# Performance work log

Hardware: AMD Instinct MI355X
Metric: run time of the kernel (lower is better)

## Reference

```python
import jax, jax.numpy as jnp
import numpy as np

B, S, HID = 1, 2048, 4096
H, KV, D = 32, 8, 128          # query heads, kv heads, head_dim
THETA = 100000.0               # rope base


def setup_inputs() -> dict:
    key = jax.random.key(0)
    k1, k2, k3, k4, k5 = jax.random.split(key, 5)
    hidden_states = jax.random.normal(k1, (B, S, HID), jnp.float32)
    # W_pack: Linear(hidden, H*D + 2*KV*D), torch weight layout [out, in]
    w_pack = jax.random.normal(k2, (H * D + 2 * KV * D, HID), jnp.float32) * 0.02
    w_o = jax.random.normal(k3, (HID, H * D), jnp.float32) * 0.02
    # conv kernels: per-kv-head causal mixing weights of width 2 (softmax-normalized at init)
    conv_k = jax.nn.softmax(jax.random.normal(k4, (KV, 2), jnp.float32), axis=-1)
    conv_v = jax.nn.softmax(jax.random.normal(k5, (KV, 2), jnp.float32), axis=-1)
    return dict(hidden_states=hidden_states, w_pack=w_pack, w_o=w_o,
                conv_k=conv_k, conv_v=conv_v)


def _causal_conv2(u, k):
    """u: [b,s,h,d], k: [h,2]. v[t] = k[h,0]*u[t-1] + k[h,1]*u[t] (zero pad at t=-1).
    Equivalent to custom_convolution with window 2 (unfold+mul+sum)."""
    prev = jnp.pad(u, ((0, 0), (1, 0), (0, 0), (0, 0)))[:, :-1]
    return k[None, None, :, 0:1] * prev + k[None, None, :, 1:2] * u


def _rope(x):
    """Non-interleaved (half-split) rotary over full head_dim. x: [b,s,h,d]."""
    s, d = x.shape[1], x.shape[-1]
    inv = 1.0 / (THETA ** (jnp.arange(0, d, 2, dtype=jnp.float32) / d))
    freqs = jnp.arange(s, dtype=jnp.float32)[:, None] * inv[None, :]  # [s, d/2]
    cos = jnp.cos(freqs)[None, :, None, :]
    sin = jnp.sin(freqs)[None, :, None, :]
    x1, x2 = x[..., : d // 2], x[..., d // 2:]
    return jnp.concatenate([x1 * cos - x2 * sin, x1 * sin + x2 * cos], axis=-1)


def reference(hidden_states, w_pack, w_o, conv_k, conv_v):
    qkv = hidden_states @ w_pack.T                       # [b,s,H*D+2*KV*D]
    q = qkv[..., : H * D].reshape(B, S, H, D)
    k = qkv[..., H * D: H * D + KV * D].reshape(B, S, KV, D)
    v = qkv[..., H * D + KV * D:].reshape(B, S, KV, D)

    # causal depthwise width-2 conv mixing on K and V (prefill path)
    k = _causal_conv2(k, conv_k)
    v = _causal_conv2(v, conv_v)

    # rotary on q, k
    q = _rope(q)
    k = _rope(k)

    # GQA: repeat kv heads to match query heads
    g = H // KV
    k = jnp.repeat(k, g, axis=2)
    v = jnp.repeat(v, g, axis=2)

    scale = 1.0 / np.sqrt(D).astype(np.float32)
    scores = jnp.einsum('bqhd,bkhd->bhqk', q, k) * scale  # [b,H,S,S]
    causal = jnp.tril(jnp.ones((S, S), dtype=bool))
    scores = jnp.where(causal[None, None], scores, jnp.finfo(scores.dtype).min)
    probs = jax.nn.softmax(scores, axis=-1)
    out = jnp.einsum('bhqk,bkhd->bqhd', probs, v).reshape(B, S, H * D)
    return out @ w_o.T
```

## Files before the change

kernel.cpp:

```cpp
#include <hip/hip_runtime.h>
#include <hip/hip_bf16.h>

#define S_LEN 2048
#define HID 4096
#define NH 32
#define NKV 8
#define HD 128

typedef unsigned short u16;
typedef __attribute__((ext_vector_type(4))) float f32x4;
typedef __attribute__((ext_vector_type(8))) short bf16x8;

__device__ __forceinline__ u16 f2bf(float x) {
  union { float f; unsigned u; } c; c.f = x;
  unsigned r = c.u + 0x7FFFu + ((c.u >> 16) & 1u);
  return (u16)(r >> 16);
}

__device__ __forceinline__ void gload16(const void* g, void* l) {
  __builtin_amdgcn_global_load_lds(
      (const __attribute__((address_space(1))) unsigned int*)g,
      (__attribute__((address_space(3))) unsigned int*)l, 16, 0, 0);
}

__global__ void cvt4_kernel(const float* __restrict__ s, u16* __restrict__ d, int n4) {
  int i = blockIdx.x * 256 + threadIdx.x;
  if (i >= n4) return;
  float4 v = ((const float4*)s)[i];
  ushort4 o;
  o.x = f2bf(v.x); o.y = f2bf(v.y); o.z = f2bf(v.z); o.w = f2bf(v.w);
  ((ushort4*)d)[i] = o;
}

__global__ void rope_tab_kernel(float2* __restrict__ tab) {
  int i = blockIdx.x * 256 + threadIdx.x;
  int t = i >> 6, d = i & 63;
  float inv = expf(-(float)d * (11.512925464970229f / 64.0f));
  float f = (float)t * inv;
  float2 cs; cs.x = cosf(f); cs.y = sinf(f);
  tab[i] = cs;
}

__global__ void rope_q_kernel(const float* __restrict__ qkv, const float2* __restrict__ tab,
                              u16* __restrict__ Q) {
  int i = blockIdx.x * 256 + threadIdx.x;
  int d = i & 63, h = (i >> 6) & 31, t = i >> 11;
  const float* row = qkv + (size_t)t * 6144 + h * 128;
  float x1 = row[d], x2 = row[d + 64];
  float2 cs = tab[(t << 6) | d];
  u16* orow = Q + (((size_t)t * NH + h) << 7);
  orow[d]      = f2bf(x1 * cs.x - x2 * cs.y);
  orow[d + 64] = f2bf(x1 * cs.y + x2 * cs.x);
}

__global__ void convrope_k_kernel(const float* __restrict__ qkv, const float* __restrict__ ck,
                                  const float2* __restrict__ tab, u16* __restrict__ K) {
  int i = blockIdx.x * 256 + threadIdx.x;
  int d = i & 63, kv = (i >> 6) & 7, t = i >> 9;
  const float* cur = qkv + (size_t)t * 6144 + 4096 + kv * 128;
  float c0 = ck[kv * 2], c1 = ck[kv * 2 + 1];
  float x1 = c1 * cur[d], x2 = c1 * cur[d + 64];
  if (t > 0) { const float* prv = cur - 6144; x1 += c0 * prv[d]; x2 += c0 * prv[d + 64]; }
  float2 cs = tab[(t << 6) | d];
  u16* orow = K + (((size_t)t * NKV + kv) << 7);
  orow[d]      = f2bf(x1 * cs.x - x2 * cs.y);
  orow[d + 64] = f2bf(x1 * cs.y + x2 * cs.x);
}

__global__ __launch_bounds__(256) void convT_v_kernel(const float* __restrict__ qkv,
                                                      const float* __restrict__ cv,
                                                      u16* __restrict__ VT) {
  __shared__ float ld[65][128];
  int tt = blockIdx.x * 64, kv = blockIdx.y;
  float c0 = cv[kv * 2], c1 = cv[kv * 2 + 1];
  for (int idx = threadIdx.x; idx < 65 * 128; idx += 256) {
    int r = idx >> 7, d = idx & 127;
    int t = tt - 1 + r;
    ld[r][d] = (t >= 0) ? qkv[(size_t)t * 6144 + 5120 + kv * 128 + d] : 0.f;
  }
  __syncthreads();
  int d = threadIdx.x >> 1, tc = (threadIdx.x & 1) * 32;
  u16* out = VT + ((size_t)kv * 128 + d) * S_LEN + tt + tc;
#pragma unroll
  for (int j = 0; j < 32; ++j)
    out[j] = f2bf(c0 * ld[tc + j][d] + c1 * ld[tc + j + 1][d]);
}

#define BM 128
#define BN 128
#define BK 64

__global__ __launch_bounds__(256, 2) void gemm_nt_kernel(const u16* __restrict__ A,
                                                         const u16* __restrict__ B,
                                                         float* __restrict__ C,
                                                         int M, int N, int K) {
  __shared__ __align__(16) u16 lA[BM * BK];
  __shared__ __align__(16) u16 lB[BN * BK];
  const int tid = threadIdx.x;
  const int wid = tid >> 6, lane = tid & 63;
  const int bm = blockIdx.y * BM, bn = blockIdx.x * BN;
  const int wr = (wid >> 1) * 64, wc = (wid & 1) * 64;
  const int lr = lane & 15, lg = lane >> 4;
  f32x4 acc[4][4] = {};
  const char* Ab = (const char*)A;
  const char* Bb = (const char*)B;
  const int nk = K / BK;
  for (int kt = 0; kt < nk; ++kt) {
    const size_t k0b = (size_t)kt * (BK * 2);
    __syncthreads();
#pragma unroll
    for (int i = 0; i < 4; ++i) {
      int off = (i * 4 + wid) * 1024 + lane * 16;
      int row = off >> 7, inrow = off & 127;
      int sw = inrow ^ ((row & 7) << 4);
      gload16(Ab + (size_t)(bm + row) * (K * 2) + k0b + sw, (char*)lA + (i * 4 + wid) * 1024);
      gload16(Bb + (size_t)(bn + row) * (K * 2) + k0b + sw, (char*)lB + (i * 4 + wid) * 1024);
    }
    __syncthreads();
    bf16x8 af[4][2], bfv[4][2];
#pragma unroll
    for (int m = 0; m < 4; ++m)
#pragma unroll
      for (int ks = 0; ks < 2; ++ks) {
        int row = wr + m * 16 + lr;
        int boff = row * 128 + ((ks * 64 + lg * 16) ^ ((row & 7) << 4));
        af[m][ks] = *(const bf16x8*)((const char*)lA + boff);
      }
#pragma unroll
    for (int n = 0; n < 4; ++n)
#pragma unroll
      for (int ks = 0; ks < 2; ++ks) {
        int row = wc + n * 16 + lr;
        int boff = row * 128 + ((ks * 64 + lg * 16) ^ ((row & 7) << 4));
        bfv[n][ks] = *(const bf16x8*)((const char*)lB + boff);
      }
#pragma unroll
    for (int m = 0; m < 4; ++m)
#pragma unroll
      for (int n = 0; n < 4; ++n)
#pragma unroll
        for (int ks = 0; ks < 2; ++ks)
          acc[m][n] = __builtin_amdgcn_mfma_f32_16x16x32_bf16(af[m][ks], bfv[n][ks], acc[m][n], 0, 0, 0);
  }
#pragma unroll
  for (int m = 0; m < 4; ++m)
#pragma unroll
    for (int n = 0; n < 4; ++n)
#pragma unroll
      for (int r = 0; r < 4; ++r) {
        int row = bm + wr + m * 16 + lg * 4 + r;
        int col = bn + wc + n * 16 + lr;
        C[(size_t)row * N + col] = acc[m][n][r];
      }
}

__global__ __launch_bounds__(256, 2) void attn_kernel(const u16* __restrict__ Q,
                                                      const u16* __restrict__ K,
                                                      const u16* __restrict__ VT,
                                                      u16* __restrict__ O) {
  __shared__ __align__(16) u16 lK[64 * 128];
  __shared__ __align__(16) u16 lV[128 * 64];
  __shared__ __align__(16) u16 lP[4][16 * 64];
  const int tid = threadIdx.x;
  const int wid = tid >> 6, lane = tid & 63;
  const int lr = lane & 15, lg = lane >> 4;
  const int qt = blockIdx.x, h = blockIdx.y;
  const int kvh = h >> 2;
  const int qrow = qt * 64 + wid * 16 + lr;

  bf16x8 qf[4];
#pragma unroll
  for (int ks = 0; ks < 4; ++ks)
    qf[ks] = *(const bf16x8*)(Q + (((size_t)qrow * NH + h) << 7) + ks * 32 + lg * 8);

  f32x4 o[8] = {};
  float mrow[4], lrow[4];
#pragma unroll
  for (int r = 0; r < 4; ++r) { mrow[r] = -1e30f; lrow[r] = 0.f; }

  const char* Kb = (const char*)K;
  const char* Vb = (const char*)VT;
  const float SC = 0.12752551286084f;

  for (int kt = 0; kt <= qt; ++kt) {
    __syncthreads();
#pragma unroll
    for (int i = 0; i < 4; ++i) {
      int off = (i * 4 + wid) * 1024 + lane * 16;
      int t = off >> 8, inrow = off & 255;
      gload16(Kb + (((size_t)((kt * 64 + t) * NKV + kvh)) << 8) + (inrow ^ ((t & 7) << 4)),
              (char*)lK + (i * 4 + wid) * 1024);
      int d = off >> 7, inr2 = off & 127;
      gload16(Vb + ((size_t)(kvh * 128 + d)) * (S_LEN * 2) + kt * 128 + (inr2 ^ ((d & 7) << 4)),
              (char*)lV + (i * 4 + wid) * 1024);
    }
    __syncthreads();

    f32x4 sv[4];
#pragma unroll
    for (int n = 0; n < 4; ++n) {
      f32x4 a = {};
#pragma unroll
      for (int ks = 0; ks < 4; ++ks) {
        int trow = n * 16 + lr;
        int boff = trow * 256 + ((ks * 64 + lg * 16) ^ ((trow & 7) << 4));
        bf16x8 kf = *(const bf16x8*)((const char*)lK + boff);
        a = __builtin_amdgcn_mfma_f32_16x16x32_bf16(qf[ks], kf, a, 0, 0, 0);
      }
      sv[n] = a;
    }
#pragma unroll
    for (int n = 0; n < 4; ++n)
#pragma unroll
      for (int r = 0; r < 4; ++r)
        sv[n][r] *= SC;
    if (kt == qt) {
#pragma unroll
      for (int n = 0; n < 4; ++n)
#pragma unroll
        for (int r = 0; r < 4; ++r) {
          int col = n * 16 + lr, rw = wid * 16 + lg * 4 + r;
          if (col > rw) sv[n][r] = -1e30f;
        }
    }
    float pm[4];
#pragma unroll
    for (int r = 0; r < 4; ++r)
      pm[r] = fmaxf(fmaxf(sv[0][r], sv[1][r]), fmaxf(sv[2][r], sv[3][r]));
#pragma unroll
    for (int r = 0; r < 4; ++r) {
      pm[r] = fmaxf(pm[r], __shfl_xor(pm[r], 1));
      pm[r] = fmaxf(pm[r], __shfl_xor(pm[r], 2));
      pm[r] = fmaxf(pm[r], __shfl_xor(pm[r], 4));
      pm[r] = fmaxf(pm[r], __shfl_xor(pm[r], 8));
    }
    float alpha[4];
#pragma unroll
    for (int r = 0; r < 4; ++r) {
      float mn = fmaxf(mrow[r], pm[r]);
      alpha[r] = exp2f(mrow[r] - mn);
      mrow[r] = mn;
    }
    float rs[4] = {0.f, 0.f, 0.f, 0.f};
#pragma unroll
    for (int n = 0; n < 4; ++n)
#pragma unroll
      for (int r = 0; r < 4; ++r) {
        float p = exp2f(sv[n][r] - mrow[r]);
        sv[n][r] = p;
        rs[r] += p;
      }
#pragma unroll
    for (int r = 0; r < 4; ++r) {
      rs[r] += __shfl_xor(rs[r], 1);
      rs[r] += __shfl_xor(rs[r], 2);
      rs[r] += __shfl_xor(rs[r], 4);
      rs[r] += __shfl_xor(rs[r], 8);
      lrow[r] = lrow[r] * alpha[r] + rs[r];
    }
#pragma unroll
    for (int nt = 0; nt < 8; ++nt)
#pragma unroll
      for (int r = 0; r < 4; ++r)
        o[nt][r] *= alpha[r];
    char* pb = (char*)lP[wid];
#pragma unroll
    for (int n = 0; n < 4; ++n)
#pragma unroll
      for (int r = 0; r < 4; ++r) {
        int row = lg * 4 + r, col = n * 16 + lr;
        int boff = (row * 128 + col * 2) ^ ((row & 7) << 4);
        *(u16*)(pb + boff) = f2bf(sv[n][r]);
      }
#pragma unroll
    for (int ks = 0; ks < 2; ++ks) {
      int aboff = lr * 128 + ((ks * 64 + lg * 16) ^ ((lr & 7) << 4));
      bf16x8 pf = *(const bf16x8*)((const char*)pb + aboff);
#pragma unroll
      for (int nt = 0; nt < 8; ++nt) {
        int drow = nt * 16 + lr;
        int vboff = drow * 128 + ((ks * 64 + lg * 16) ^ ((drow & 7) << 4));
        bf16x8 vf = *(const bf16x8*)((const char*)lV + vboff);
        o[nt] = __builtin_amdgcn_mfma_f32_16x16x32_bf16(pf, vf, o[nt], 0, 0, 0);
      }
    }
  }
  float rinv[4];
#pragma unroll
  for (int r = 0; r < 4; ++r) rinv[r] = 1.0f / lrow[r];
#pragma unroll
  for (int nt = 0; nt < 8; ++nt)
#pragma unroll
    for (int r = 0; r < 4; ++r) {
      int row = qt * 64 + wid * 16 + lg * 4 + r;
      int col = nt * 16 + lr;
      O[(size_t)row * 4096 + h * 128 + col] = f2bf(o[nt][r] * rinv[r]);
    }
}

extern "C" void kernel_launch(void* const* d_in, const int* in_sizes, int n_in,
                              void* d_out, int out_size, void* d_ws, size_t ws_size,
                              hipStream_t stream) {
  const float* hidden = (const float*)d_in[0];
  const float* wpack  = (const float*)d_in[1];
  const float* wo     = (const float*)d_in[2];
  const float* convk  = (const float*)d_in[3];
  const float* convv  = (const float*)d_in[4];
  float* out = (float*)d_out;

  char* w = (char*)d_ws;
  u16*  hiddenB = (u16*)w;
  u16*  wpackB  = (u16*)(w + 16777216);
  float* qkv    = (float*)(w + 67108864);
  u16*  qrope   = (u16*)(w + 117440512);
  u16*  krope   = (u16*)(w + 134217728);
  u16*  vT      = (u16*)(w + 138412032);
  float2* tab   = (float2*)(w + 142606336);

  cvt4_kernel<<<8192, 256, 0, stream>>>(hidden, hiddenB, 2097152);
  cvt4_kernel<<<24576, 256, 0, stream>>>(wpack, wpackB, 6291456);
  rope_tab_kernel<<<512, 256, 0, stream>>>(tab);
  gemm_nt_kernel<<<dim3(48, 16), 256, 0, stream>>>(hiddenB, wpackB, qkv, 2048, 6144, 4096);
  cvt4_kernel<<<16384, 256, 0, stream>>>(wo, wpackB, 4194304);
  rope_q_kernel<<<16384, 256, 0, stream>>>(qkv, tab, qrope);
  convrope_k_kernel<<<4096, 256, 0, stream>>>(qkv, convk, tab, krope);
  convT_v_kernel<<<dim3(32, 8), 256, 0, stream>>>(qkv, convv, vT);
  attn_kernel<<<dim3(32, 32), 256, 0, stream>>>(qrope, krope, vT, hiddenB);
  gemm_nt_kernel<<<dim3(32, 16), 256, 0, stream>>>(hiddenB, wpackB, out, 2048, 4096, 4096);
}
```

Before: 598.2 us.

## Pair causal query tiles per block, double-buffer K/V, lazy softmax rescale

The attention kernel now handles two query tiles per block (tile i and 31-i), which balances causal work across blocks and lets both tiles share each staged K/V tile. K/V loads are double-buffered so the next tile's global-to-LDS copy overlaps compute on the current one. The scaling factor is folded into Q during RoPE, and the online-softmax rescale of the output is skipped unless the running max grows by more than a threshold. In exchange, the grid halves to 512 blocks, LDS and register use roughly double, and the lazy rescale allows unnormalized values to grow to about 2^8 before correction.

```diff
diff --git a/kernel.cpp b/kernel.cpp
--- a/kernel.cpp
+++ b/kernel.cpp
@@ -48,9 +48,10 @@
   const float* row = qkv + (size_t)t * 6144 + h * 128;
   float x1 = row[d], x2 = row[d + 64];
   float2 cs = tab[(t << 6) | d];
+  const float SC = 0.12752551286084f;
   u16* orow = Q + (((size_t)t * NH + h) << 7);
-  orow[d]      = f2bf(x1 * cs.x - x2 * cs.y);
-  orow[d + 64] = f2bf(x1 * cs.y + x2 * cs.x);
+  orow[d]      = f2bf((x1 * cs.x - x2 * cs.y) * SC);
+  orow[d + 64] = f2bf((x1 * cs.y + x2 * cs.x) * SC);
 }
 
 __global__ void convrope_k_kernel(const float* __restrict__ qkv, const float* __restrict__ ck,
@@ -158,44 +159,54 @@
                                                       const u16* __restrict__ K,
                                                       const u16* __restrict__ VT,
                                                       u16* __restrict__ O) {
-  __shared__ __align__(16) u16 lK[64 * 128];
-  __shared__ __align__(16) u16 lV[128 * 64];
+  __shared__ __align__(16) u16 lK[2][64 * 128];
+  __shared__ __align__(16) u16 lV[2][128 * 64];
   __shared__ __align__(16) u16 lP[4][16 * 64];
   const int tid = threadIdx.x;
   const int wid = tid >> 6, lane = tid & 63;
   const int lr = lane & 15, lg = lane >> 4;
-  const int qt = blockIdx.x, h = blockIdx.y;
+  const int q0 = blockIdx.x, h = blockIdx.y;
   const int kvh = h >> 2;
-  const int qrow = qt * 64 + wid * 16 + lr;
-
-  bf16x8 qf[4];
-#pragma unroll
-  for (int ks = 0; ks < 4; ++ks)
-    qf[ks] = *(const bf16x8*)(Q + (((size_t)qrow * NH + h) << 7) + ks * 32 + lg * 8);
-
-  f32x4 o[8] = {};
-  float mrow[4], lrow[4];
-#pragma unroll
-  for (int r = 0; r < 4; ++r) { mrow[r] = -1e30f; lrow[r] = 0.f; }
+  const int qtA = q0, qtB = 31 - q0;
+
+  bf16x8 qfA[4], qfB[4];
+  {
+    const int rA = qtA * 64 + wid * 16 + lr;
+    const int rB = qtB * 64 + wid * 16 + lr;
+#pragma unroll
+    for (int ks = 0; ks < 4; ++ks) {
+      qfA[ks] = *(const bf16x8*)(Q + (((size_t)rA * NH + h) << 7) + ks * 32 + lg * 8);
+      qfB[ks] = *(const bf16x8*)(Q + (((size_t)rB * NH + h) << 7) + ks * 32 + lg * 8);
+    }
+  }
+
+  f32x4 oA[8] = {}, oB[8] = {};
+  float mA[4], lsA[4], mB[4], lsB[4];
+#pragma unroll
+  for (int r = 0; r < 4; ++r) { mA[r] = mB[r] = -1e30f; lsA[r] = lsB[r] = 0.f; }
 
   const char* Kb = (const char*)K;
   const char* Vb = (const char*)VT;
-  const float SC = 0.12752551286084f;
-
-  for (int kt = 0; kt <= qt; ++kt) {
-    __syncthreads();
+  char* pb = (char*)lP[wid];
+
+  auto stage = [&](int buf, int kt) {
+    char* dK = (char*)lK[buf];
+    char* dV = (char*)lV[buf];
 #pragma unroll
     for (int i = 0; i < 4; ++i) {
       int off = (i * 4 + wid) * 1024 + lane * 16;
       int t = off >> 8, inrow = off & 255;
       gload16(Kb + (((size_t)((kt * 64 + t) * NKV + kvh)) << 8) + (inrow ^ ((t & 7) << 4)),
-              (char*)lK + (i * 4 + wid) * 1024);
+              dK + (i * 4 + wid) * 1024);
       int d = off >> 7, inr2 = off & 127;
       gload16(Vb + ((size_t)(kvh * 128 + d)) * (S_LEN * 2) + kt * 128 + (inr2 ^ ((d & 7) << 4)),
-              (char*)lV + (i * 4 + wid) * 1024);
-    }
-    __syncthreads();
-
+              dV + (i * 4 + wid) * 1024);
+    }
+  };
+
+  auto step = [&](const bf16x8* qf, f32x4* o, float* mrow, float* lrow, int buf, bool diag) {
+    const char* kb = (const char*)lK[buf];
+    const char* vb = (const char*)lV[buf];
     f32x4 sv[4];
 #pragma unroll
     for (int n = 0; n < 4; ++n) {
@@ -204,17 +215,12 @@
       for (int ks = 0; ks < 4; ++ks) {
         int trow = n * 16 + lr;
         int boff = trow * 256 + ((ks * 64 + lg * 16) ^ ((trow & 7) << 4));
-        bf16x8 kf = *(const bf16x8*)((const char*)lK + boff);
+        bf16x8 kf = *(const bf16x8*)(kb + boff);
         a = __builtin_amdgcn_mfma_f32_16x16x32_bf16(qf[ks], kf, a, 0, 0, 0);
       }
       sv[n] = a;
     }
-#pragma unroll
-    for (int n = 0; n < 4; ++n)
-#pragma unroll
-      for (int r = 0; r < 4; ++r)
-        sv[n][r] *= SC;
-    if (kt == qt) {
+    if (diag) {
 #pragma unroll
       for (int n = 0; n < 4; ++n)
 #pragma unroll
@@ -234,12 +240,18 @@
       pm[r] = fmaxf(pm[r], __shfl_xor(pm[r], 4));
       pm[r] = fmaxf(pm[r], __shfl_xor(pm[r], 8));
     }
-    float alpha[4];
-#pragma unroll
-    for (int r = 0; r < 4; ++r) {
-      float mn = fmaxf(mrow[r], pm[r]);
-      alpha[r] = exp2f(mrow[r] - mn);
-      mrow[r] = mn;
+    bool need = (pm[0] > mrow[0] + 8.f) | (pm[1] > mrow[1] + 8.f) |
+                (pm[2] > mrow[2] + 8.f) | (pm[3] > mrow[3] + 8.f);
+    if (__any(need)) {
+#pragma unroll
+      for (int r = 0; r < 4; ++r) {
+        float mn = fmaxf(mrow[r], pm[r]);
+        float al = exp2f(mrow[r] - mn);
+        mrow[r] = mn;
+        lrow[r] *= al;
+#pragma unroll
+        for (int nt = 0; nt < 8; ++nt) o[nt][r] *= al;
+      }
     }
     float rs[4] = {0.f, 0.f, 0.f, 0.f};
 #pragma unroll
@@ -247,8 +259,10 @@
 #pragma unroll
       for (int r = 0; r < 4; ++r) {
         float p = exp2f(sv[n][r] - mrow[r]);
-        sv[n][r] = p;
         rs[r] += p;
+        int row = lg * 4 + r, col = n * 16 + lr;
+        int boff = (row * 128 + col * 2) ^ ((row & 7) << 4);
+        *(u16*)(pb + boff) = f2bf(p);
       }
 #pragma unroll
     for (int r = 0; r < 4; ++r) {
@@ -256,45 +270,43 @@
       rs[r] += __shfl_xor(rs[r], 2);
       rs[r] += __shfl_xor(rs[r], 4);
       rs[r] += __shfl_xor(rs[r], 8);
-      lrow[r] = lrow[r] * alpha[r] + rs[r];
-    }
-#pragma unroll
-    for (int nt = 0; nt < 8; ++nt)
-#pragma unroll
-      for (int r = 0; r < 4; ++r)
-        o[nt][r] *= alpha[r];
-    char* pb = (char*)lP[wid];
-#pragma unroll
-    for (int n = 0; n < 4; ++n)
-#pragma unroll
-      for (int r = 0; r < 4; ++r) {
-        int row = lg * 4 + r, col = n * 16 + lr;
-        int boff = (row * 128 + col * 2) ^ ((row & 7) << 4);
-        *(u16*)(pb + boff) = f2bf(sv[n][r]);
-      }
+      lrow[r] += rs[r];
+    }
 #pragma unroll
     for (int ks = 0; ks < 2; ++ks) {
       int aboff = lr * 128 + ((ks * 64 + lg * 16) ^ ((lr & 7) << 4));
-      bf16x8 pf = *(const bf16x8*)((const char*)pb + aboff);
+      bf16x8 pf = *(const bf16x8*)(pb + aboff);
 #pragma unroll
       for (int nt = 0; nt < 8; ++nt) {
         int drow = nt * 16 + lr;
         int vboff = drow * 128 + ((ks * 64 + lg * 16) ^ ((drow & 7) << 4));
-        bf16x8 vf = *(const bf16x8*)((const char*)lV + vboff);
+        bf16x8 vf = *(const bf16x8*)(vb + vboff);
         o[nt] = __builtin_amdgcn_mfma_f32_16x16x32_bf16(pf, vf, o[nt], 0, 0, 0);
       }
     }
+  };
+
+  stage(0, 0);
+  __syncthreads();
+  for (int kt = 0; kt <= qtB; ++kt) {
+    int cur = kt & 1;
+    if (kt < qtB) stage(cur ^ 1, kt + 1);
+    if (kt <= qtA) step(qfA, oA, mA, lsA, cur, kt == qtA);
+    step(qfB, oB, mB, lsB, cur, kt == qtB);
+    __syncthreads();
   }
-  float rinv[4];
-#pragma unroll
-  for (int r = 0; r < 4; ++r) rinv[r] = 1.0f / lrow[r];
+
+#pragma unroll
+  for (int r = 0; r < 4; ++r) { lsA[r] = 1.0f / lsA[r]; lsB[r] = 1.0f / lsB[r]; }
 #pragma unroll
   for (int nt = 0; nt < 8; ++nt)
 #pragma unroll
     for (int r = 0; r < 4; ++r) {
-      int row = qt * 64 + wid * 16 + lg * 4 + r;
+      int rowA = qtA * 64 + wid * 16 + lg * 4 + r;
+      int rowB = qtB * 64 + wid * 16 + lg * 4 + r;
       int col = nt * 16 + lr;
-      O[(size_t)row * 4096 + h * 128 + col] = f2bf(o[nt][r] * rinv[r]);
+      O[(size_t)rowA * 4096 + h * 128 + col] = f2bf(oA[nt][r] * lsA[r]);
+      O[(size_t)rowB * 4096 + h * 128 + col] = f2bf(oB[nt][r] * lsB[r]);
     }
 }
 
@@ -325,6 +337,6 @@
   rope_q_kernel<<<16384, 256, 0, stream>>>(qkv, tab, qrope);
   convrope_k_kernel<<<4096, 256, 0, stream>>>(qkv, convk, tab, krope);
   convT_v_kernel<<<dim3(32, 8), 256, 0, stream>>>(qkv, convv, vT);
-  attn_kernel<<<dim3(32, 32), 256, 0, stream>>>(qrope, krope, vT, hiddenB);
+  attn_kernel<<<dim3(16, 32), 256, 0, stream>>>(qrope, krope, vT, hiddenB);
   gemm_nt_kernel<<<dim3(32, 16), 256, 0, stream>>>(hiddenB, wpackB, out, 2048, 4096, 4096);
 }
```

New measurement: 530.2 us. 1.13x faster.
